# Performance work log

Measured on AMD Instinct MI355X. Metric: run time of the kernel, lower is better.

## Reference

```python
import jax, jax.numpy as jnp
import numpy as np

B, S, D = 2, 2048, 2048
H = 16
Q_LORA, KV_LORA = 1536, 512
D_NOPE, D_ROPE, D_V = 128, 64, 128
D_QK = D_NOPE + D_ROPE  # 192
EPS = 1e-6


def rmsnorm(x, w):
    return x * jax.lax.rsqrt(jnp.mean(x * x, axis=-1, keepdims=True) + EPS) * w


def apply_rope(x, freqs_cis):
    # x: (B, S, h, D_ROPE); freqs_cis: (S, D_ROPE//2, 2) = (cos, sin)
    # DeepSeek pairs consecutive elements (2i, 2i+1) as complex re/im.
    b, s, h, d = x.shape
    xp = x.reshape(b, s, h, d // 2, 2)
    re, im = xp[..., 0], xp[..., 1]
    cos = freqs_cis[None, :, None, :, 0]
    sin = freqs_cis[None, :, None, :, 1]
    out_re = re * cos - im * sin
    out_im = re * sin + im * cos
    return jnp.stack([out_re, out_im], axis=-1).reshape(b, s, h, d)


def setup_inputs() -> dict:
    key = jax.random.key(0)
    ks = jax.random.split(key, 8)
    sd = 0.02
    x = jax.random.normal(ks[0], (B, S, D), dtype=jnp.float32)
    # RoPE table over the rope head dim
    inv_freq = 1.0 / (10000.0 ** (np.arange(0, D_ROPE, 2, dtype=np.float32) / D_ROPE))
    t = np.arange(S, dtype=np.float32)
    f = np.outer(t, inv_freq)  # (S, 32)
    freqs_cis = jnp.asarray(np.stack([np.cos(f), np.sin(f)], axis=-1), dtype=jnp.float32)
    return {
        "x": x,
        "start_pos": 0,
        "freqs_cis": freqs_cis,
        "wq_a": jax.random.normal(ks[1], (Q_LORA, D), dtype=jnp.float32) * sd,
        "q_norm_w": jnp.ones((Q_LORA,), dtype=jnp.float32),
        "wq_b": jax.random.normal(ks[2], (H * D_QK, Q_LORA), dtype=jnp.float32) * sd,
        "wkv_a": jax.random.normal(ks[3], (KV_LORA + D_ROPE, D), dtype=jnp.float32) * sd,
        "kv_norm_w": jnp.ones((KV_LORA,), dtype=jnp.float32),
        "wkv_b": jax.random.normal(ks[4], (H * (D_NOPE + D_V), KV_LORA), dtype=jnp.float32) * sd,
        "wo": jax.random.normal(ks[5], (D, H * D_V), dtype=jnp.float32) * sd,
    }


def reference(x, start_pos, freqs_cis, wq_a, q_norm_w, wq_b, wkv_a, kv_norm_w, wkv_b, wo):
    bsz, seqlen, _ = x.shape
    softmax_scale = D_QK ** (-0.5)

    # --- queries: low-rank down-proj, RMSNorm, up-proj ---
    q = rmsnorm(x @ wq_a.T, q_norm_w) @ wq_b.T          # (B,S,H*D_QK)
    q = q.reshape(bsz, seqlen, H, D_QK)
    q_nope, q_pe = q[..., :D_NOPE], q[..., D_NOPE:]
    q_pe = apply_rope(q_pe, freqs_cis)
    q = jnp.concatenate([q_nope, q_pe], axis=-1)         # (B,S,H,192)

    # --- keys/values: compressed latent + shared rope key ---
    kv = x @ wkv_a.T                                     # (B,S,KV_LORA+D_ROPE)
    kv_c, k_pe = kv[..., :KV_LORA], kv[..., KV_LORA:]
    k_pe = apply_rope(k_pe[:, :, None, :], freqs_cis)    # (B,S,1,64)
    kvb = rmsnorm(kv_c, kv_norm_w) @ wkv_b.T             # (B,S,H*(D_NOPE+D_V))
    kvb = kvb.reshape(bsz, seqlen, H, D_NOPE + D_V)
    k_nope, v = kvb[..., :D_NOPE], kvb[..., D_NOPE:]
    k = jnp.concatenate([k_nope, jnp.broadcast_to(k_pe, (bsz, seqlen, H, D_ROPE))], axis=-1)

    # --- causal attention (FA2 with attention_mask=None) ---
    scores = jnp.einsum("bqhd,bkhd->bhqk", q, k) * softmax_scale
    causal = jnp.tril(jnp.ones((seqlen, seqlen), dtype=bool))
    scores = jnp.where(causal[None, None], scores, jnp.finfo(scores.dtype).min)
    attn = jax.nn.softmax(scores, axis=-1)
    out = jnp.einsum("bhqk,bkhd->bqhd", attn, v)         # (B,S,H,D_V)
    # (v padding to qk_head_dim then slicing [..., :D_V] is a no-op)
    return out.reshape(bsz, seqlen, H * D_V) @ wo.T
```

## Files before the change

kernel.cpp:

```cpp
#include <hip/hip_runtime.h>
#include <math.h>

typedef short short8 __attribute__((ext_vector_type(8)));
typedef float float4v __attribute__((ext_vector_type(4)));
#define AS1 __attribute__((address_space(1)))
#define AS3 __attribute__((address_space(3)))

__device__ __forceinline__ float b2f(ushort u) {
    unsigned v = ((unsigned)u) << 16; float f; __builtin_memcpy(&f, &v, 4); return f;
}
__device__ __forceinline__ ushort f2b(float f) {
    unsigned v; __builtin_memcpy(&v, &f, 4);
    unsigned r = (v + 0x7fffu + ((v >> 16) & 1u)) >> 16;
    return (ushort)r;
}

__global__ void cvt_pad(const float* __restrict__ src, ushort* __restrict__ dst,
                        int src_rows, int cols, int total4, float scl) {
    int i = blockIdx.x * 256 + threadIdx.x;
    if (i >= total4) return;
    size_t e = (size_t)i * 4;
    int r = (int)(e / (size_t)cols);
    ushort4 o;
    if (r < src_rows) {
        float4 v = *(const float4*)(src + e);
        o.x = f2b(v.x * scl); o.y = f2b(v.y * scl); o.z = f2b(v.z * scl); o.w = f2b(v.w * scl);
    } else {
        o.x = 0; o.y = 0; o.z = 0; o.w = 0;
    }
    *(ushort4*)(dst + e) = o;
}

__device__ __forceinline__ short8 rdf(const ushort* base, int row, int kb) {
    int raw = row * 128 + kb;
    int off = raw ^ (((raw >> 9) & 1) << 5);
    return *(const short8*)((const char*)base + off);
}
__device__ __forceinline__ void stage_half(const ushort* __restrict__ G, int ldg,
                                           int row0, int k0, ushort* ldsbase,
                                           int wave, int lane) {
#pragma unroll
    for (int rr = 0; rr < 2; ++rr) {
        int x = rr * 8192 + wave * 1024 + lane * 16;
        int l = x ^ (((x >> 9) & 1) << 5);
        int r = l >> 7, c2 = l & 127;
        __builtin_amdgcn_global_load_lds(
            (const AS1 void*)(G + (size_t)(row0 + r) * ldg + k0 + (c2 >> 1)),
            (AS3 void*)((char*)ldsbase + rr * 8192 + wave * 1024), 16, 0, 0);
    }
}

#define GBAR() do { asm volatile("" ::: "memory"); __builtin_amdgcn_s_barrier(); } while (0)

#define PHASE(QD, SB, VMTAIL, ...) do {                                               \
    short8 a0  = rdf(&sA[SB][0], wm * 128 + (2 * (QD)) * 16 + lq, quad * 16);         \
    short8 a0k = rdf(&sA[SB][0], wm * 128 + (2 * (QD)) * 16 + lq, 64 + quad * 16);    \
    short8 a1  = rdf(&sA[SB][0], wm * 128 + (2 * (QD) + 1) * 16 + lq, quad * 16);     \
    short8 a1k = rdf(&sA[SB][0], wm * 128 + (2 * (QD) + 1) * 16 + lq, 64 + quad * 16);\
    if ((QD) == 0) {                                                                  \
        _Pragma("unroll")                                                             \
        for (int fc = 0; fc < 4; ++fc) {                                              \
            bF[fc][0] = rdf(&sB[SB][0], wn * 64 + fc * 16 + lq, quad * 16);           \
            bF[fc][1] = rdf(&sB[SB][0], wn * 64 + fc * 16 + lq, 64 + quad * 16);      \
        }                                                                             \
    }                                                                                 \
    __VA_ARGS__;                                                                      \
    GBAR();                                                                           \
    __builtin_amdgcn_s_setprio(1);                                                    \
    _Pragma("unroll")                                                                 \
    for (int fc = 0; fc < 4; ++fc) {                                                  \
        acc[2*(QD)][fc]   = __builtin_amdgcn_mfma_f32_16x16x32_bf16(a0,  bF[fc][0], acc[2*(QD)][fc],   0, 0, 0); \
        acc[2*(QD)][fc]   = __builtin_amdgcn_mfma_f32_16x16x32_bf16(a0k, bF[fc][1], acc[2*(QD)][fc],   0, 0, 0); \
        acc[2*(QD)+1][fc] = __builtin_amdgcn_mfma_f32_16x16x32_bf16(a1,  bF[fc][0], acc[2*(QD)+1][fc], 0, 0, 0); \
        acc[2*(QD)+1][fc] = __builtin_amdgcn_mfma_f32_16x16x32_bf16(a1k, bF[fc][1], acc[2*(QD)+1][fc], 0, 0, 0); \
    }                                                                                 \
    __builtin_amdgcn_s_setprio(0);                                                    \
    VMTAIL;                                                                           \
    GBAR();                                                                           \
} while (0)

__global__ __launch_bounds__(512, 2)
void gemm8p(const ushort* __restrict__ A, const ushort* __restrict__ B,
            void* __restrict__ Cv, int K, int lda, int ldb, int ldc, int mode,
            int nbn, int ncol, ushort* __restrict__ Kf, ushort* __restrict__ Vtp) {
    __shared__ ushort sA[2][256 * 64];
    __shared__ ushort sB[2][256 * 64];
    const int tid = threadIdx.x, wave = tid >> 6, lane = tid & 63;
    const int lq = lane & 15, quad = lane >> 4;
    const int wm = wave >> 2, wn = wave & 3;
    const int nwg = gridDim.x;
    const int wg = (blockIdx.x & 7) * (nwg >> 3) + (blockIdx.x >> 3);
    const int bm = (wg / nbn) * 256, bn = (wg % nbn) * 256;

    ushort* sA0h0 = &sA[0][0];     ushort* sA0h1 = &sA[0][8192];
    ushort* sA1h0 = &sA[1][0];     ushort* sA1h1 = &sA[1][8192];
    ushort* sB0h0 = &sB[0][0];     ushort* sB0h1 = &sB[0][8192];
    ushort* sB1h0 = &sB[1][0];     ushort* sB1h1 = &sB[1][8192];

    float4v acc[8][4] = {};
    const int nkt = K >> 6;
    const int iters = nkt >> 1;

    stage_half(A, lda, bm,       0, sA0h0, wave, lane);
    stage_half(A, lda, bm + 128, 0, sA0h1, wave, lane);
    stage_half(B, ldb, bn,       0, sB0h0, wave, lane);
    stage_half(B, ldb, bn + 128, 0, sB0h1, wave, lane);
    stage_half(B, ldb, bn,      64, sB1h0, wave, lane);
    stage_half(B, ldb, bn + 128,64, sB1h1, wave, lane);
    asm volatile("s_waitcnt vmcnt(4)" ::: "memory");
    GBAR();

    for (int j = 0; j < iters; ++j) {
        const int t1 = 2 * j + 1, t2 = 2 * j + 2, t3 = 2 * j + 3;
        const bool lastj = (j == iters - 1);
        short8 bF[4][2];
        PHASE(0, 0, (void)0, stage_half(A, lda, bm,       t1 * 64, sA1h0, wave, lane));
        PHASE(1, 0, (void)0, stage_half(A, lda, bm + 128, t1 * 64, sA1h1, wave, lane));
        PHASE(2, 0, (void)0, if (t2 < nkt) stage_half(B, ldb, bn,       t2 * 64, sB0h0, wave, lane));
        PHASE(3, 0,
              if (lastj) { asm volatile("s_waitcnt vmcnt(0)" ::: "memory"); }
              else       { asm volatile("s_waitcnt vmcnt(4)" ::: "memory"); },
              if (t2 < nkt) stage_half(B, ldb, bn + 128, t2 * 64, sB0h1, wave, lane));
        PHASE(0, 1, (void)0, if (t2 < nkt) stage_half(A, lda, bm,       t2 * 64, sA0h0, wave, lane));
        PHASE(1, 1, (void)0, if (t2 < nkt) stage_half(A, lda, bm + 128, t2 * 64, sA0h1, wave, lane));
        PHASE(2, 1, (void)0, if (t3 < nkt) stage_half(B, ldb, bn,       t3 * 64, sB1h0, wave, lane));
        PHASE(3, 1,
              if (lastj) { asm volatile("s_waitcnt vmcnt(0)" ::: "memory"); }
              else       { asm volatile("s_waitcnt vmcnt(4)" ::: "memory"); },
              if (t3 < nkt) stage_half(B, ldb, bn + 128, t3 * 64, sB1h1, wave, lane));
    }

#pragma unroll
    for (int fr = 0; fr < 8; ++fr) {
        int row0 = bm + wm * 128 + fr * 16 + quad * 4;
#pragma unroll
        for (int fc = 0; fc < 4; ++fc) {
            int col = bn + wn * 64 + fc * 16 + lq;
            if (mode == 0) {
                if (col < ncol) {
                    ushort* C = (ushort*)Cv;
#pragma unroll
                    for (int r = 0; r < 4; ++r)
                        C[(size_t)(row0 + r) * ldc + col] = f2b(acc[fr][fc][r]);
                }
            } else if (mode == 1) {
                if (col < ncol) {
                    float* C = (float*)Cv;
#pragma unroll
                    for (int r = 0; r < 4; ++r)
                        C[(size_t)(row0 + r) * ldc + col] = acc[fr][fc][r];
                }
            } else {
                int h = col >> 8, c = col & 255;
                int bh = ((row0 >> 11) << 4) + h;
                if (c < 128) {
#pragma unroll
                    for (int r = 0; r < 4; ++r) {
                        int s = (row0 + r) & 2047;
                        Kf[((size_t)bh * 2048 + s) * 200 + c] = f2b(acc[fr][fc][r]);
                    }
                } else {
                    int d = c - 128;
                    int kt = (row0 & 2047) >> 6, kv = row0 & 63;
                    ushort4 o;
                    o.x = f2b(acc[fr][fc][0]); o.y = f2b(acc[fr][fc][1]);
                    o.z = f2b(acc[fr][fc][2]); o.w = f2b(acc[fr][fc][3]);
                    *(ushort4*)(Vtp + (((size_t)bh * 32 + kt) * 128 + d) * 72 + kv) = o;
                }
            }
        }
    }
}

__global__ void rmsnorm_inplace(ushort* __restrict__ d, const float* __restrict__ w,
                                int cols, int ld) {
    int row = blockIdx.x, tid = threadIdx.x;
    ushort* p = d + (size_t)row * ld;
    float ss = 0.f;
    for (int i = tid; i < cols; i += 256) { float v = b2f(p[i]); ss += v * v; }
#pragma unroll
    for (int off = 32; off >= 1; off >>= 1) ss += __shfl_xor(ss, off);
    __shared__ float red[4];
    if ((tid & 63) == 0) red[tid >> 6] = ss;
    __syncthreads();
    float tot = red[0] + red[1] + red[2] + red[3];
    float rs = rsqrtf(tot / (float)cols + 1e-6f);
    for (int i = tid; i < cols; i += 256) p[i] = f2b(b2f(p[i]) * rs * w[i]);
}

__global__ void kvnorm_rope(const ushort* __restrict__ kvraw, const float* __restrict__ w,
                            const float* __restrict__ freqs, ushort* __restrict__ kvc,
                            ushort* __restrict__ kpe, int ld) {
    int row = blockIdx.x, tid = threadIdx.x;
    int s = row & 2047;
    const ushort* p = kvraw + (size_t)row * ld;
    float v0 = b2f(p[tid]), v1 = b2f(p[tid + 256]);
    float ss = v0 * v0 + v1 * v1;
#pragma unroll
    for (int off = 32; off >= 1; off >>= 1) ss += __shfl_xor(ss, off);
    __shared__ float red[4];
    if ((tid & 63) == 0) red[tid >> 6] = ss;
    __syncthreads();
    float tot = red[0] + red[1] + red[2] + red[3];
    float rs = rsqrtf(tot / 512.f + 1e-6f);
    kvc[(size_t)row * 512 + tid] = f2b(v0 * rs * w[tid]);
    kvc[(size_t)row * 512 + tid + 256] = f2b(v1 * rs * w[tid + 256]);
    if (tid < 32) {
        float re = b2f(p[512 + 2 * tid]), im = b2f(p[512 + 2 * tid + 1]);
        float cs = freqs[(s * 32 + tid) * 2], sn = freqs[(s * 32 + tid) * 2 + 1];
        kpe[(size_t)row * 64 + 2 * tid] = f2b(re * cs - im * sn);
        kpe[(size_t)row * 64 + 2 * tid + 1] = f2b(re * sn + im * cs);
    }
}

__global__ void qrope(ushort* __restrict__ q, const float* __restrict__ freqs) {
    int idx = blockIdx.x * 256 + threadIdx.x;
    int i = idx & 31;
    int h = (idx >> 5) & 15;
    int srow = idx >> 9;
    int s = srow & 2047;
    ushort* p = q + ((size_t)srow * 16 + h) * 192 + 128 + 2 * i;
    float re = b2f(p[0]), im = b2f(p[1]);
    float cs = freqs[(s * 32 + i) * 2], sn = freqs[(s * 32 + i) * 2 + 1];
    p[0] = f2b(re * cs - im * sn);
    p[1] = f2b(re * sn + im * cs);
}

__global__ void kpe_fill(const ushort* __restrict__ kpe, ushort* __restrict__ Kfull) {
    int tid = threadIdx.x;
    int row = blockIdx.x * 8 + (tid >> 5);
    int c = tid & 31;
    int bh = row >> 11, s = row & 2047, b = bh >> 4;
    ushort2 v;
    v.x = kpe[((size_t)b * 2048 + s) * 64 + 2 * c];
    v.y = kpe[((size_t)b * 2048 + s) * 64 + 2 * c + 1];
    *(ushort2*)(Kfull + (size_t)row * 200 + 128 + 2 * c) = v;
}

__global__ __launch_bounds__(512, 2)
void mla_attn13(const ushort* __restrict__ q, const ushort* __restrict__ Kfull,
                const ushort* __restrict__ Vt, ushort* __restrict__ out) {
    __shared__ ushort sK[128 * 200];
    __shared__ ushort sP[8][16][72];
    const int tid = threadIdx.x, wave = tid >> 6, lane = tid & 63;
    const int lq = lane & 15, quad = lane >> 4;
    const int lin = blockIdx.x;
    const int e = lin & 7, idx = lin >> 3;
    const int st = 15 - (idx >> 2);
    const int bh = e + 8 * (idx & 3);
    const int b = bh >> 4, h = bh & 15;
    const ushort* Kb = Kfull + (size_t)bh * 2048 * 200;
    const ushort* Vb = Vt + (size_t)bh * 32 * 128 * 72;

    const int qrow = st * 128 + wave * 16 + lq;
    const ushort* qp = q + ((size_t)(b * 2048 + qrow) * 16 + h) * 192 + quad * 8;
    short8 qf[6];
#pragma unroll
    for (int c = 0; c < 6; ++c) qf[c] = *(const short8*)(qp + c * 32);

    float4v oacc[8] = {};
    float m_i[4] = {-INFINITY, -INFINITY, -INFINITY, -INFINITY};
    float l_i[4] = {0.f, 0.f, 0.f, 0.f};
    const int myrow0 = st * 128 + wave * 16 + quad * 4;

    for (int kt = 0; kt <= st; ++kt) {
        const ushort* Ksrc = Kb + (size_t)kt * 128 * 200;
#pragma unroll
        for (int i = 0; i < 7; ++i) {
            int cb = i * 512 + wave * 64;
            if (cb < 3200)
                __builtin_amdgcn_global_load_lds((const AS1 void*)(Ksrc + (size_t)(cb + lane) * 8),
                                                 (AS3 void*)(sK + cb * 8), 16, 0, 0);
        }
        __syncthreads();
        const ushort* Vs0 = Vb + (size_t)(2 * kt) * 128 * 72 + (size_t)lq * 72 + quad * 8;
        const ushort* Vs1 = Vs0 + 128 * 72;
        float4v sc[8];
#pragma unroll
        for (int ct = 0; ct < 8; ++ct) {
            float4v a = {0.f, 0.f, 0.f, 0.f};
#pragma unroll
            for (int c = 0; c < 6; ++c) {
                short8 kf = *(const short8*)(sK + (ct * 16 + lq) * 200 + c * 32 + quad * 8);
                a = __builtin_amdgcn_mfma_f32_16x16x32_bf16(qf[c], kf, a, 0, 0, 0);
            }
            sc[ct] = a;
        }
        short8 vf00[8];
#pragma unroll
        for (int dt = 0; dt < 8; ++dt)
            vf00[dt] = *(const short8*)(Vs0 + (size_t)dt * 16 * 72);
        float mnew[4];
#pragma unroll
        for (int r = 0; r < 4; ++r) mnew[r] = m_i[r];
#pragma unroll
        for (int ct = 0; ct < 8; ++ct)
#pragma unroll
            for (int r = 0; r < 4; ++r) {
                float v = (kt * 128 + ct * 16 + lq) > (myrow0 + r) ? -INFINITY : sc[ct][r];
                sc[ct][r] = v;
                mnew[r] = fmaxf(mnew[r], v);
            }
#pragma unroll
        for (int off = 8; off >= 1; off >>= 1)
#pragma unroll
            for (int r = 0; r < 4; ++r) mnew[r] = fmaxf(mnew[r], __shfl_xor(mnew[r], off));
        float g = mnew[0] - m_i[0];
#pragma unroll
        for (int r = 1; r < 4; ++r) g = fmaxf(g, mnew[r] - m_i[r]);
        if (__ballot(g > 8.0f) != 0ull) {
#pragma unroll
            for (int r = 0; r < 4; ++r) {
                float a = __builtin_amdgcn_exp2f(m_i[r] - mnew[r]);
                m_i[r] = mnew[r];
                l_i[r] *= a;
#pragma unroll
                for (int dt = 0; dt < 8; ++dt) oacc[dt][r] *= a;
            }
        }
        float psum[4] = {0.f, 0.f, 0.f, 0.f};
#pragma unroll
        for (int c4 = 0; c4 < 4; ++c4)
#pragma unroll
            for (int r = 0; r < 4; ++r) {
                float pv = __builtin_amdgcn_exp2f(sc[c4][r] - m_i[r]);
                psum[r] += pv;
                sP[wave][quad * 4 + r][c4 * 16 + lq] = f2b(pv);
            }
#pragma unroll
        for (int kc = 0; kc < 2; ++kc) {
            short8 pf = *(const short8*)(&sP[wave][lq][kc * 32 + quad * 8]);
#pragma unroll
            for (int dt = 0; dt < 8; ++dt) {
                short8 vf = kc == 0 ? vf00[dt]
                                    : *(const short8*)(Vs0 + (size_t)dt * 16 * 72 + 32);
                oacc[dt] = __builtin_amdgcn_mfma_f32_16x16x32_bf16(pf, vf, oacc[dt], 0, 0, 0);
            }
        }
#pragma unroll
        for (int c4 = 0; c4 < 4; ++c4)
#pragma unroll
            for (int r = 0; r < 4; ++r) {
                float pv = __builtin_amdgcn_exp2f(sc[4 + c4][r] - m_i[r]);
                psum[r] += pv;
                sP[wave][quad * 4 + r][c4 * 16 + lq] = f2b(pv);
            }
#pragma unroll
        for (int kc = 0; kc < 2; ++kc) {
            short8 pf = *(const short8*)(&sP[wave][lq][kc * 32 + quad * 8]);
#pragma unroll
            for (int dt = 0; dt < 8; ++dt) {
                short8 vf = *(const short8*)(Vs1 + (size_t)dt * 16 * 72 + kc * 32);
                oacc[dt] = __builtin_amdgcn_mfma_f32_16x16x32_bf16(pf, vf, oacc[dt], 0, 0, 0);
            }
        }
#pragma unroll
        for (int off = 8; off >= 1; off >>= 1)
#pragma unroll
            for (int r = 0; r < 4; ++r) psum[r] += __shfl_xor(psum[r], off);
#pragma unroll
        for (int r = 0; r < 4; ++r) l_i[r] += psum[r];
        __syncthreads();
    }
    float inv[4];
#pragma unroll
    for (int r = 0; r < 4; ++r) inv[r] = 1.f / l_i[r];
#pragma unroll
    for (int dt = 0; dt < 8; ++dt) {
#pragma unroll
        for (int r = 0; r < 4; ++r) {
            out[((size_t)(b * 2048 + myrow0 + r) * 16 + h) * 128 + dt * 16 + lq] =
                f2b(oacc[dt][r] * inv[r]);
        }
    }
}

extern "C" void kernel_launch(void* const* d_in, const int* in_sizes, int n_in,
                              void* d_out, int out_size, void* d_ws, size_t ws_size,
                              hipStream_t stream) {
    const float* x     = (const float*)d_in[0];
    const float* freqs = (const float*)d_in[2];
    const float* wq_a  = (const float*)d_in[3];
    const float* qnw   = (const float*)d_in[4];
    const float* wq_b  = (const float*)d_in[5];
    const float* wkv_a = (const float*)d_in[6];
    const float* kvnw  = (const float*)d_in[7];
    const float* wkv_b = (const float*)d_in[8];
    const float* wo    = (const float*)d_in[9];

    char* ws = (char*)d_ws;
    size_t off = 0;
    auto alloc = [&](size_t n) { char* p = ws + off; off += (n + 255) & ~(size_t)255; return p; };
    ushort* xb    = (ushort*)alloc(4096ull * 2048 * 2);
    ushort* wqkva = (ushort*)alloc(2304ull * 2048 * 2);
    ushort* wqbb  = (ushort*)alloc(3072ull * 1536 * 2);
    ushort* wkvbb = (ushort*)alloc(4096ull * 512 * 2);
    ushort* wob   = (ushort*)alloc(2048ull * 2048 * 2);
    ushort* qakv  = (ushort*)alloc(4096ull * 2176 * 2);
    ushort* kvc   = (ushort*)alloc(4096ull * 512 * 2);
    ushort* kpe   = (ushort*)alloc(4096ull * 64 * 2);
    ushort* qfull = (ushort*)alloc(4096ull * 3072 * 2);
    ushort* kvbuf = (ushort*)alloc(4096ull * 4096 * 2);
    ushort* attno = (ushort*)alloc(4096ull * 2048 * 2);
    if (off > ws_size) return;
    ushort* Kfull = kvbuf;
    ushort* Vt = xb;

    auto cvt = [&](const float* s, ushort* dd, int sr, int cols, size_t dtot, float scl) {
        int t4 = (int)(dtot / 4);
        cvt_pad<<<(t4 + 255) / 256, 256, 0, stream>>>(s, dd, sr, cols, t4, scl);
    };
    const float qk_scale = 1.44269504f / sqrtf(192.0f);
    cvt(x, xb, 4096, 2048, 4096ull * 2048, 1.f);
    cvt(wq_a, wqkva, 1536, 2048, 1536ull * 2048, 1.f);
    cvt(wkv_a, wqkva + 1536ull * 2048, 576, 2048, 768ull * 2048, 1.f);
    cvt(wq_b, wqbb, 3072, 1536, 3072ull * 1536, qk_scale);
    cvt(wkv_b, wkvbb, 4096, 512, 4096ull * 512, 1.f);
    cvt(wo, wob, 2048, 2048, 2048ull * 2048, 1.f);

    gemm8p<<<dim3(144), 512, 0, stream>>>(xb, wqkva, qakv, 2048, 2048, 2048, 2176, 0, 9, 2176, nullptr, nullptr);
    rmsnorm_inplace<<<4096, 256, 0, stream>>>(qakv, qnw, 1536, 2176);
    kvnorm_rope<<<4096, 256, 0, stream>>>(qakv + 1536, kvnw, freqs, kvc, kpe, 2176);
    gemm8p<<<dim3(192), 512, 0, stream>>>(qakv, wqbb, qfull, 1536, 2176, 1536, 3072, 0, 12, 3072, nullptr, nullptr);
    qrope<<<8192, 256, 0, stream>>>(qfull, freqs);
    kpe_fill<<<8192, 256, 0, stream>>>(kpe, Kfull);
    gemm8p<<<dim3(256), 512, 0, stream>>>(kvc, wkvbb, nullptr, 512, 512, 512, 0, 2, 16, 0, Kfull, Vt);
    mla_attn13<<<dim3(512), 512, 0, stream>>>(qfull, Kfull, Vt, attno);
    gemm8p<<<dim3(128), 512, 0, stream>>>(attno, wob, (float*)d_out, 2048, 2048, 2048, 2048, 1, 8, 2048, nullptr, nullptr);
}
```

Before: 474.4 us.

## Fuse conversions, norms, q-RoPE and k_pe fill to cut kernel launches

Six separate fp32-to-bf16 conversion launches become one kernel that dispatches on block index. The q and kv RMSNorm kernels are merged, and the kv RoPE result is written directly into the per-head Kfull layout, which drops the kpe_fill kernel. Query RoPE moves into the wq_b GEMM epilogue (new mode 3) using a lane shuffle to fetch the paired element, which removes the qrope pass over qfull. The aim is fewer launches and fewer global round trips, at the cost of more branching and extra freqs loads in the GEMM epilogue.

```diff
diff --git a/kernel.cpp b/kernel.cpp
--- a/kernel.cpp
+++ b/kernel.cpp
@@ -15,11 +15,22 @@
     return (ushort)r;
 }
 
-__global__ void cvt_pad(const float* __restrict__ src, ushort* __restrict__ dst,
-                        int src_rows, int cols, int total4, float scl) {
-    int i = blockIdx.x * 256 + threadIdx.x;
-    if (i >= total4) return;
-    size_t e = (size_t)i * 4;
+__global__ void cvt_all(const float* __restrict__ s0, ushort* __restrict__ d0,
+                        const float* __restrict__ s1, ushort* __restrict__ d1,
+                        const float* __restrict__ s2, ushort* __restrict__ d2,
+                        const float* __restrict__ s3, ushort* __restrict__ d3,
+                        const float* __restrict__ s4, ushort* __restrict__ d4,
+                        const float* __restrict__ s5, ushort* __restrict__ d5,
+                        float scl3) {
+    int bid = blockIdx.x;
+    const float* src; ushort* dst; int src_rows, cols; float scl = 1.f;
+    if (bid < 8192)       {              src = s0; dst = d0; src_rows = 4096; cols = 2048; }
+    else if (bid < 11264) { bid -= 8192; src = s1; dst = d1; src_rows = 1536; cols = 2048; }
+    else if (bid < 12800) { bid -= 11264; src = s2; dst = d2; src_rows = 576;  cols = 2048; }
+    else if (bid < 17408) { bid -= 12800; src = s3; dst = d3; src_rows = 3072; cols = 1536; scl = scl3; }
+    else if (bid < 19456) { bid -= 17408; src = s4; dst = d4; src_rows = 4096; cols = 512; }
+    else                  { bid -= 19456; src = s5; dst = d5; src_rows = 2048; cols = 2048; }
+    size_t e = ((size_t)bid * 256 + threadIdx.x) * 4;
     int r = (int)(e / (size_t)cols);
     ushort4 o;
     if (r < src_rows) {
@@ -82,7 +93,8 @@
 __global__ __launch_bounds__(512, 2)
 void gemm8p(const ushort* __restrict__ A, const ushort* __restrict__ B,
             void* __restrict__ Cv, int K, int lda, int ldb, int ldc, int mode,
-            int nbn, int ncol, ushort* __restrict__ Kf, ushort* __restrict__ Vtp) {
+            int nbn, int ncol, ushort* __restrict__ Kf, ushort* __restrict__ Vtp,
+            const float* __restrict__ freqs) {
     __shared__ ushort sA[2][256 * 64];
     __shared__ ushort sB[2][256 * 64];
     const int tid = threadIdx.x, wave = tid >> 6, lane = tid & 63;
@@ -150,6 +162,25 @@
                     for (int r = 0; r < 4; ++r)
                         C[(size_t)(row0 + r) * ldc + col] = acc[fr][fc][r];
                 }
+            } else if (mode == 3) {
+                ushort* C = (ushort*)Cv;
+                int d = col % 192;
+                bool pe = d >= 128;
+                bool odd = (col & 1) != 0;
+#pragma unroll
+                for (int r = 0; r < 4; ++r) {
+                    float v = acc[fr][fc][r];
+                    float pr = __shfl_xor(v, 1);
+                    float outv = v;
+                    if (pe) {
+                        int i2 = (d - 128) >> 1;
+                        int s = (row0 + r) & 2047;
+                        float cs = freqs[((size_t)s * 32 + i2) * 2];
+                        float sn = freqs[((size_t)s * 32 + i2) * 2 + 1];
+                        outv = odd ? (pr * sn + v * cs) : (v * cs - pr * sn);
+                    }
+                    C[(size_t)(row0 + r) * ldc + col] = f2b(outv);
+                }
             } else {
                 int h = col >> 8, c = col & 255;
                 int bh = ((row0 >> 11) << 4) + h;
@@ -172,69 +203,44 @@
     }
 }
 
-__global__ void rmsnorm_inplace(ushort* __restrict__ d, const float* __restrict__ w,
-                                int cols, int ld) {
-    int row = blockIdx.x, tid = threadIdx.x;
-    ushort* p = d + (size_t)row * ld;
+__global__ void norm_fused(ushort* __restrict__ qakv, const float* __restrict__ qnw,
+                           const float* __restrict__ kvnw, const float* __restrict__ freqs,
+                           ushort* __restrict__ kvc, ushort* __restrict__ Kfull) {
+    const int row = blockIdx.x, tid = threadIdx.x;
+    const int s = row & 2047, b = row >> 11;
+    __shared__ float red[4];
+    __shared__ ushort kvpe[64];
+    ushort* p = qakv + (size_t)row * 2176;
     float ss = 0.f;
-    for (int i = tid; i < cols; i += 256) { float v = b2f(p[i]); ss += v * v; }
+    for (int i = tid; i < 1536; i += 256) { float v = b2f(p[i]); ss += v * v; }
 #pragma unroll
     for (int off = 32; off >= 1; off >>= 1) ss += __shfl_xor(ss, off);
-    __shared__ float red[4];
     if ((tid & 63) == 0) red[tid >> 6] = ss;
     __syncthreads();
-    float tot = red[0] + red[1] + red[2] + red[3];
-    float rs = rsqrtf(tot / (float)cols + 1e-6f);
-    for (int i = tid; i < cols; i += 256) p[i] = f2b(b2f(p[i]) * rs * w[i]);
-}
-
-__global__ void kvnorm_rope(const ushort* __restrict__ kvraw, const float* __restrict__ w,
-                            const float* __restrict__ freqs, ushort* __restrict__ kvc,
-                            ushort* __restrict__ kpe, int ld) {
-    int row = blockIdx.x, tid = threadIdx.x;
-    int s = row & 2047;
-    const ushort* p = kvraw + (size_t)row * ld;
-    float v0 = b2f(p[tid]), v1 = b2f(p[tid + 256]);
-    float ss = v0 * v0 + v1 * v1;
-#pragma unroll
-    for (int off = 32; off >= 1; off >>= 1) ss += __shfl_xor(ss, off);
-    __shared__ float red[4];
-    if ((tid & 63) == 0) red[tid >> 6] = ss;
+    float rs = rsqrtf((red[0] + red[1] + red[2] + red[3]) / 1536.f + 1e-6f);
+    for (int i = tid; i < 1536; i += 256) p[i] = f2b(b2f(p[i]) * rs * qnw[i]);
     __syncthreads();
-    float tot = red[0] + red[1] + red[2] + red[3];
-    float rs = rsqrtf(tot / 512.f + 1e-6f);
-    kvc[(size_t)row * 512 + tid] = f2b(v0 * rs * w[tid]);
-    kvc[(size_t)row * 512 + tid + 256] = f2b(v1 * rs * w[tid + 256]);
+    const ushort* pk = p + 1536;
+    float v0 = b2f(pk[tid]), v1 = b2f(pk[tid + 256]);
+    float s2 = v0 * v0 + v1 * v1;
+#pragma unroll
+    for (int off = 32; off >= 1; off >>= 1) s2 += __shfl_xor(s2, off);
+    if ((tid & 63) == 0) red[tid >> 6] = s2;
+    __syncthreads();
+    float rs2 = rsqrtf((red[0] + red[1] + red[2] + red[3]) / 512.f + 1e-6f);
+    kvc[(size_t)row * 512 + tid] = f2b(v0 * rs2 * kvnw[tid]);
+    kvc[(size_t)row * 512 + tid + 256] = f2b(v1 * rs2 * kvnw[tid + 256]);
     if (tid < 32) {
-        float re = b2f(p[512 + 2 * tid]), im = b2f(p[512 + 2 * tid + 1]);
+        float re = b2f(pk[512 + 2 * tid]), im = b2f(pk[512 + 2 * tid + 1]);
         float cs = freqs[(s * 32 + tid) * 2], sn = freqs[(s * 32 + tid) * 2 + 1];
-        kpe[(size_t)row * 64 + 2 * tid] = f2b(re * cs - im * sn);
-        kpe[(size_t)row * 64 + 2 * tid + 1] = f2b(re * sn + im * cs);
-    }
-}
-
-__global__ void qrope(ushort* __restrict__ q, const float* __restrict__ freqs) {
-    int idx = blockIdx.x * 256 + threadIdx.x;
-    int i = idx & 31;
-    int h = (idx >> 5) & 15;
-    int srow = idx >> 9;
-    int s = srow & 2047;
-    ushort* p = q + ((size_t)srow * 16 + h) * 192 + 128 + 2 * i;
-    float re = b2f(p[0]), im = b2f(p[1]);
-    float cs = freqs[(s * 32 + i) * 2], sn = freqs[(s * 32 + i) * 2 + 1];
-    p[0] = f2b(re * cs - im * sn);
-    p[1] = f2b(re * sn + im * cs);
-}
-
-__global__ void kpe_fill(const ushort* __restrict__ kpe, ushort* __restrict__ Kfull) {
-    int tid = threadIdx.x;
-    int row = blockIdx.x * 8 + (tid >> 5);
-    int c = tid & 31;
-    int bh = row >> 11, s = row & 2047, b = bh >> 4;
-    ushort2 v;
-    v.x = kpe[((size_t)b * 2048 + s) * 64 + 2 * c];
-    v.y = kpe[((size_t)b * 2048 + s) * 64 + 2 * c + 1];
-    *(ushort2*)(Kfull + (size_t)row * 200 + 128 + 2 * c) = v;
+        kvpe[2 * tid]     = f2b(re * cs - im * sn);
+        kvpe[2 * tid + 1] = f2b(re * sn + im * cs);
+    }
+    __syncthreads();
+    int h = tid >> 4, c4 = (tid & 15) * 4;
+    ushort4 v;
+    v.x = kvpe[c4]; v.y = kvpe[c4 + 1]; v.z = kvpe[c4 + 2]; v.w = kvpe[c4 + 3];
+    *(ushort4*)(Kfull + ((size_t)(b * 16 + h) * 2048 + s) * 200 + 128 + c4) = v;
 }
 
 __global__ __launch_bounds__(512, 2)
@@ -403,28 +409,18 @@
     ushort* kvbuf = (ushort*)alloc(4096ull * 4096 * 2);
     ushort* attno = (ushort*)alloc(4096ull * 2048 * 2);
     if (off > ws_size) return;
+    (void)kpe;
     ushort* Kfull = kvbuf;
     ushort* Vt = xb;
 
-    auto cvt = [&](const float* s, ushort* dd, int sr, int cols, size_t dtot, float scl) {
-        int t4 = (int)(dtot / 4);
-        cvt_pad<<<(t4 + 255) / 256, 256, 0, stream>>>(s, dd, sr, cols, t4, scl);
-    };
     const float qk_scale = 1.44269504f / sqrtf(192.0f);
-    cvt(x, xb, 4096, 2048, 4096ull * 2048, 1.f);
-    cvt(wq_a, wqkva, 1536, 2048, 1536ull * 2048, 1.f);
-    cvt(wkv_a, wqkva + 1536ull * 2048, 576, 2048, 768ull * 2048, 1.f);
-    cvt(wq_b, wqbb, 3072, 1536, 3072ull * 1536, qk_scale);
-    cvt(wkv_b, wkvbb, 4096, 512, 4096ull * 512, 1.f);
-    cvt(wo, wob, 2048, 2048, 2048ull * 2048, 1.f);
-
-    gemm8p<<<dim3(144), 512, 0, stream>>>(xb, wqkva, qakv, 2048, 2048, 2048, 2176, 0, 9, 2176, nullptr, nullptr);
-    rmsnorm_inplace<<<4096, 256, 0, stream>>>(qakv, qnw, 1536, 2176);
-    kvnorm_rope<<<4096, 256, 0, stream>>>(qakv + 1536, kvnw, freqs, kvc, kpe, 2176);
-    gemm8p<<<dim3(192), 512, 0, stream>>>(qakv, wqbb, qfull, 1536, 2176, 1536, 3072, 0, 12, 3072, nullptr, nullptr);
-    qrope<<<8192, 256, 0, stream>>>(qfull, freqs);
-    kpe_fill<<<8192, 256, 0, stream>>>(kpe, Kfull);
-    gemm8p<<<dim3(256), 512, 0, stream>>>(kvc, wkvbb, nullptr, 512, 512, 512, 0, 2, 16, 0, Kfull, Vt);
+    cvt_all<<<dim3(23552), 256, 0, stream>>>(x, xb, wq_a, wqkva,
+                                             wkv_a, wqkva + 1536ull * 2048,
+                                             wq_b, wqbb, wkv_b, wkvbb, wo, wob, qk_scale);
+    gemm8p<<<dim3(144), 512, 0, stream>>>(xb, wqkva, qakv, 2048, 2048, 2048, 2176, 0, 9, 2176, nullptr, nullptr, nullptr);
+    norm_fused<<<dim3(4096), 256, 0, stream>>>(qakv, qnw, kvnw, freqs, kvc, Kfull);
+    gemm8p<<<dim3(192), 512, 0, stream>>>(qakv, wqbb, qfull, 1536, 2176, 1536, 3072, 3, 12, 3072, nullptr, nullptr, freqs);
+    gemm8p<<<dim3(256), 512, 0, stream>>>(kvc, wkvbb, nullptr, 512, 512, 512, 0, 2, 16, 0, Kfull, Vt, nullptr);
     mla_attn13<<<dim3(512), 512, 0, stream>>>(qfull, Kfull, Vt, attno);
-    gemm8p<<<dim3(128), 512, 0, stream>>>(attno, wob, (float*)d_out, 2048, 2048, 2048, 2048, 1, 8, 2048, nullptr, nullptr);
-}
+    gemm8p<<<dim3(128), 512, 0, stream>>>(attno, wob, (float*)d_out, 2048, 2048, 2048, 2048, 1, 8, 2048, nullptr, nullptr, nullptr);
+}
```

Result: no change. 478.7 us (+0.9%).
